# Performance work log

Measured on AMD Instinct MI355X. Metric: run time of the kernel, lower is better.

## Reference

```python
import jax, jax.numpy as jnp
import numpy as np

ROPE_FREQ = 100.0

def _rope1d(tok, pos, freq):
    # tok: [B, H, N, D] (D even), pos: [B, N] int positions
    D = tok.shape[-1]
    inv_freq = 1.0 / (freq ** (jnp.arange(0, D, 2, dtype=jnp.float32) / D))  # [D/2]
    ang = pos[:, None, :, None].astype(jnp.float32) * inv_freq  # [B,1,N,D/2]
    cos = jnp.concatenate([jnp.cos(ang), jnp.cos(ang)], axis=-1).astype(tok.dtype)
    sin = jnp.concatenate([jnp.sin(ang), jnp.sin(ang)], axis=-1).astype(tok.dtype)
    x1, x2 = jnp.split(tok, 2, axis=-1)
    rot = jnp.concatenate([-x2, x1], axis=-1)  # rotate_half
    return tok * cos + rot * sin

def _rope2d(tok, pos2d, freq=ROPE_FREQ):
    # tok: [B, H, N, D]; first half of D encodes y (pos2d[...,0]), second half x (pos2d[...,1])
    y, x = jnp.split(tok, 2, axis=-1)
    y = _rope1d(y, pos2d[..., 0], freq)
    x = _rope1d(x, pos2d[..., 1], freq)
    return jnp.concatenate([y, x], axis=-1)

def setup_inputs() -> dict:
    key = jax.random.key(0)
    B, N, D, Hh = 2, 2048, 768, 12
    ks = jax.random.split(key, 8)
    x = jax.random.normal(ks[0], (B, N, D), dtype=jnp.float32)
    pos2d = jax.random.randint(ks[1], (B, N, 2), 0, 64)
    rope_mask = jax.random.randint(ks[2], (B, N), 0, 2).astype(jnp.bool_)
    s = 1.0 / np.sqrt(D)
    qkv_w = jax.random.normal(ks[3], (3 * D, D), dtype=jnp.float32) * s
    qkv_b = jnp.zeros((3 * D,), dtype=jnp.float32)
    proj_w = jax.random.normal(ks[4], (D, D), dtype=jnp.float32) * s
    proj_b = jnp.zeros((D,), dtype=jnp.float32)
    return {"x": x, "qkv_w": qkv_w, "qkv_b": qkv_b, "proj_w": proj_w,
            "proj_b": proj_b, "pos2d": pos2d, "rope_mask": rope_mask}

def reference(x, qkv_w, qkv_b, proj_w, proj_b, pos2d, rope_mask):
    B, N, C = x.shape
    num_heads = 12
    head_dim = C // num_heads
    scale = head_dim ** -0.5
    qkv = x @ qkv_w.T + qkv_b  # [B,N,3C]
    qkv = qkv.reshape(B, N, 3, num_heads, head_dim).transpose(2, 0, 3, 1, 4)
    q, k, v = qkv[0], qkv[1], qkv[2]  # each [B,H,N,hd]
    q_rope = _rope2d(q, pos2d)
    k_rope = _rope2d(k, pos2d)
    mask = rope_mask[:, None, :, None]  # [B,1,N,1]
    q = jnp.where(mask, q_rope, q)
    k = jnp.where(mask, k_rope, k)
    attn = jnp.einsum('bhqd,bhkd->bhqk', q, k) * scale
    attn = jax.nn.softmax(attn, axis=-1)
    out = jnp.einsum('bhqk,bhkd->bhqd', attn, v)
    out = out.transpose(0, 2, 1, 3).reshape(B, N, C)
    out = out @ proj_w.T + proj_b
    return out
```

## Files before the change

kernel.cpp:

```cpp
#include <hip/hip_runtime.h>
#include <stdint.h>

#define B_  2
#define N_  2048
#define C_  768
#define H_  12
#define NT  (B_*N_)
#define C3  (3*C_)

typedef _Float16 h8 __attribute__((ext_vector_type(8)));
typedef _Float16 h4 __attribute__((ext_vector_type(4)));
typedef float    f4 __attribute__((ext_vector_type(4)));

__device__ __forceinline__ void gload16(const void* g, void* l) {
  __builtin_amdgcn_global_load_lds((const __attribute__((address_space(1))) void*)g,
                                   (__attribute__((address_space(3))) void*)l,
                                   16, 0, 0);
}

__global__ __launch_bounds__(256) void cvt3(const float* __restrict__ x,
                                            const float* __restrict__ w1,
                                            const float* __restrict__ w2,
                                            _Float16* __restrict__ xo,
                                            _Float16* __restrict__ w1o,
                                            _Float16* __restrict__ w2o) {
  const int NX8  = NT*C_/8;
  const int NW18 = C3*C_/8;
  int c = blockIdx.x*256 + threadIdx.x;
  const float* s; _Float16* d; int off;
  if (c < NX8)            { s = x;  d = xo;  off = c; }
  else if (c < NX8+NW18)  { s = w1; d = w1o; off = c - NX8; }
  else                    { s = w2; d = w2o; off = c - NX8 - NW18; }
  f4 a = *(const f4*)(s + (size_t)off*8);
  f4 b = *(const f4*)(s + (size_t)off*8 + 4);
  h8 o;
#pragma unroll
  for (int j = 0; j < 4; ++j) { o[j] = (_Float16)a[j]; o[j+4] = (_Float16)b[j]; }
  *(h8*)(d + (size_t)off*8) = o;
}

__global__ __launch_bounds__(256) void gemm_bt(const _Float16* __restrict__ A,
                                               const _Float16* __restrict__ W,
                                               const float* __restrict__ bias,
                                               _Float16* __restrict__ Ch,
                                               float* __restrict__ Cf,
                                               int M, int N, int K) {
  __shared__ _Float16 Alds[128*32];
  __shared__ _Float16 Wlds[128*32];
  const int tid = threadIdx.x, lane = tid & 63, w = tid >> 6;
  const int m0 = blockIdx.y*128, n0 = blockIdx.x*128;
  const int wm = w >> 1, wn = w & 1;
  const int fr = lane & 15, fq = lane >> 4;

  f4 acc[4][4] = {};

  const int c0 = tid, c1 = tid + 256;
  const _Float16* Ag0 = A + (size_t)(m0 + (c0>>2))*K + (c0&3)*8;
  const _Float16* Ag1 = A + (size_t)(m0 + (c1>>2))*K + (c1&3)*8;
  const _Float16* Wg0 = W + (size_t)(n0 + (c0>>2))*K + (c0&3)*8;
  const _Float16* Wg1 = W + (size_t)(n0 + (c1>>2))*K + (c1&3)*8;
  _Float16* Al0 = Alds + (w*64)*8;
  _Float16* Al1 = Alds + (256 + w*64)*8;
  _Float16* Wl0 = Wlds + (w*64)*8;
  _Float16* Wl1 = Wlds + (256 + w*64)*8;

  for (int kk = 0; kk < K; kk += 32) {
    gload16(Ag0 + kk, Al0);
    gload16(Ag1 + kk, Al1);
    gload16(Wg0 + kk, Wl0);
    gload16(Wg1 + kk, Wl1);
    __syncthreads();
    h8 af[4], wf[4];
#pragma unroll
    for (int mt = 0; mt < 4; ++mt)
      af[mt] = *(const h8*)&Alds[(wm*64 + mt*16 + fr)*32 + fq*8];
#pragma unroll
    for (int nt = 0; nt < 4; ++nt)
      wf[nt] = *(const h8*)&Wlds[(wn*64 + nt*16 + fr)*32 + fq*8];
#pragma unroll
    for (int mt = 0; mt < 4; ++mt)
#pragma unroll
      for (int nt = 0; nt < 4; ++nt)
        acc[mt][nt] = __builtin_amdgcn_mfma_f32_16x16x32_f16(af[mt], wf[nt], acc[mt][nt], 0, 0, 0);
    __syncthreads();
  }

#pragma unroll
  for (int nt = 0; nt < 4; ++nt) {
    const int col = n0 + wn*64 + nt*16 + fr;
    const float bv = bias[col];
#pragma unroll
    for (int mt = 0; mt < 4; ++mt) {
      const int row = m0 + wm*64 + mt*16 + fq*4;
#pragma unroll
      for (int j = 0; j < 4; ++j) {
        const float v = acc[mt][nt][j] + bv;
        if (Ch) Ch[(size_t)(row+j)*N + col] = (_Float16)v;
        else    Cf[(size_t)(row+j)*N + col] = v;
      }
    }
  }
}

__global__ __launch_bounds__(256) void rope_scatter(const _Float16* __restrict__ QKV,
                                                    const int* __restrict__ pos2d,
                                                    const void* __restrict__ maskraw,
                                                    _Float16* __restrict__ Q,
                                                    _Float16* __restrict__ Kd,
                                                    _Float16* __restrict__ Vt) {
  const int tid = threadIdx.x;
  __shared__ int sflags;
  if (tid == 0) sflags = 0;
  __syncthreads();
  const unsigned char* mbytes = (const unsigned char*)maskraw;
  int fl = 0;
#pragma unroll
  for (int k2 = 0; k2 < 16; ++k2) {
    unsigned char v = mbytes[tid*16 + k2];
    if (v == 0x3f) fl |= 1;
    if ((k2 & 3) && v) fl |= 2;
  }
  if (fl) atomicOr(&sflags, fl);
  __syncthreads();
  const int mode = (sflags & 1) ? 2 : ((sflags & 2) ? 1 : 0);

  const int g  = blockIdx.x*256 + tid;
  const int bh = g >> 11;
  const int n  = g & 2047;
  const int b  = bh / H_, h = bh % H_;
  const int t  = b*N_ + n;

  bool msk;
  if (mode == 1)      msk = mbytes[t] != 0;
  else if (mode == 0) msk = ((const int*)maskraw)[t] != 0;
  else                msk = ((const float*)maskraw)[t] != 0.0f;

  const float py = (float)pos2d[t*2 + 0];
  const float px = (float)pos2d[t*2 + 1];

  const _Float16* row = QKV + (size_t)t*C3 + h*64;
  h8 qv[8], kv[8], vv[8];
#pragma unroll
  for (int c = 0; c < 8; ++c) {
    qv[c] = *(const h8*)&row[c*8];
    kv[c] = *(const h8*)&row[C_   + c*8];
    vv[c] = *(const h8*)&row[2*C_ + c*8];
  }
  h8 qo[8], ko[8];
#pragma unroll
  for (int i = 0; i < 16; ++i) {
    const float invf = exp2f((float)i * -0.4152410118f);
    float sy, cy, sx, cx;
    __sincosf(py * invf, &sy, &cy);
    __sincosf(px * invf, &sx, &cx);
    {
      float a = (float)qv[i>>3][i&7], bq = (float)qv[(i+16)>>3][(i+16)&7];
      float r1 = msk ? (a*cy - bq*sy) : a;
      float r2 = msk ? (bq*cy + a*sy) : bq;
      qo[i>>3][i&7]           = (_Float16)(r1 * 0.125f);
      qo[(i+16)>>3][(i+16)&7] = (_Float16)(r2 * 0.125f);
      float ak = (float)kv[i>>3][i&7], bk = (float)kv[(i+16)>>3][(i+16)&7];
      float s1 = msk ? (ak*cy - bk*sy) : ak;
      float s2 = msk ? (bk*cy + ak*sy) : bk;
      ko[i>>3][i&7]           = (_Float16)s1;
      ko[(i+16)>>3][(i+16)&7] = (_Float16)s2;
    }
    {
      float a = (float)qv[(i+32)>>3][(i+32)&7], bq = (float)qv[(i+48)>>3][(i+48)&7];
      float r1 = msk ? (a*cx - bq*sx) : a;
      float r2 = msk ? (bq*cx + a*sx) : bq;
      qo[(i+32)>>3][(i+32)&7] = (_Float16)(r1 * 0.125f);
      qo[(i+48)>>3][(i+48)&7] = (_Float16)(r2 * 0.125f);
      float ak = (float)kv[(i+32)>>3][(i+32)&7], bk = (float)kv[(i+48)>>3][(i+48)&7];
      float s1 = msk ? (ak*cx - bk*sx) : ak;
      float s2 = msk ? (bk*cx + ak*sx) : bk;
      ko[(i+32)>>3][(i+32)&7] = (_Float16)s1;
      ko[(i+48)>>3][(i+48)&7] = (_Float16)s2;
    }
  }
  _Float16* Qrow = Q  + ((size_t)bh*N_ + n)*64;
  _Float16* Krow = Kd + ((size_t)bh*N_ + n)*64;
#pragma unroll
  for (int c = 0; c < 8; ++c) { *(h8*)&Qrow[c*8] = qo[c]; *(h8*)&Krow[c*8] = ko[c]; }
  _Float16* Vb = Vt + (size_t)bh*64*N_ + n;
#pragma unroll
  for (int d = 0; d < 64; ++d) Vb[(size_t)d*N_] = vv[d>>3][d&7];
}

#define KSPLIT 2
__global__ __launch_bounds__(256) void attn(const _Float16* __restrict__ Q,
                                            const _Float16* __restrict__ K,
                                            const _Float16* __restrict__ Vt,
                                            _Float16* __restrict__ Opart,
                                            float* __restrict__ lpart) {
  __shared__ _Float16 Klds[2][64*64];
  __shared__ _Float16 Vlds[2][64*64];
  __shared__ _Float16 Plds[4][32*64];
  const int tid = threadIdx.x, lane = tid & 63, w = tid >> 6;
  const int fr = lane & 15, fq = lane >> 4;
  const int bh = blockIdx.y;
  const int q0 = blockIdx.x * 128;
  const int kb0 = blockIdx.z * (N_/KSPLIT), kb1 = kb0 + N_/KSPLIT;
  const _Float16* Qb = Q  + (size_t)bh*N_*64;
  const _Float16* Kb = K  + (size_t)bh*N_*64;
  const _Float16* Vb = Vt + (size_t)bh*64*N_;

  h8 qf[2][2];
#pragma unroll
  for (int mt = 0; mt < 2; ++mt)
#pragma unroll
    for (int ks = 0; ks < 2; ++ks)
      qf[mt][ks] = *(const h8*)&Qb[(size_t)(q0 + w*32 + mt*16 + fr)*64 + ks*32 + fq*8];

  f4 o[2][4] = {};
  float l_r[2] = {};

  const int sr_l = lane >> 3;
  const int scsw = ((lane & 7) ^ sr_l) * 8;
#define STAGE(buf, kb)                                                          \
  {                                                                             \
    _Float16* kl = &Klds[buf][(w*64)*8];                                        \
    _Float16* vl = &Vlds[buf][(w*64)*8];                                        \
    int r0 = w*8 + sr_l;                                                        \
    gload16(Kb + (size_t)((kb) + r0)*64 + scsw,      kl);                       \
    gload16(Vb + (size_t)r0*N_ + (kb) + scsw,        vl);                       \
    gload16(Kb + (size_t)((kb) + 32 + r0)*64 + scsw, kl + 256*8);               \
    gload16(Vb + (size_t)(32 + r0)*N_ + (kb) + scsw, vl + 256*8);               \
  }

  STAGE(0, kb0);
  int cur = 0;
  const int xm = (fr & 7) << 3;
  _Float16* Pw = &Plds[w][0];

  for (int kb = kb0; kb < kb1; kb += 64) {
    __syncthreads();
    if (kb + 64 < kb1) STAGE(cur^1, kb + 64);

    h8 kf[4][2];
#pragma unroll
    for (int kt = 0; kt < 4; ++kt)
#pragma unroll
      for (int ks = 0; ks < 2; ++ks)
        kf[kt][ks] = *(const h8*)&Klds[cur][(kt*16 + fr)*64 + ((ks*32 + fq*8) ^ xm)];

#pragma unroll
    for (int mt = 0; mt < 2; ++mt) {
      f4 st[4];
#pragma unroll
      for (int kt = 0; kt < 4; ++kt) {
        f4 z = {0.f, 0.f, 0.f, 0.f};
        z      = __builtin_amdgcn_mfma_f32_16x16x32_f16(kf[kt][0], qf[mt][0], z, 0, 0, 0);
        st[kt] = __builtin_amdgcn_mfma_f32_16x16x32_f16(kf[kt][1], qf[mt][1], z, 0, 0, 0);
      }
      const int prow = (mt*16 + fr)*64;
      float lacc = 0.f;
#pragma unroll
      for (int kt = 0; kt < 4; ++kt) {
        float p0 = __builtin_amdgcn_exp2f(__builtin_fmaf(st[kt][0], 1.44269504f, -8.65617025f));
        float p1 = __builtin_amdgcn_exp2f(__builtin_fmaf(st[kt][1], 1.44269504f, -8.65617025f));
        float p2 = __builtin_amdgcn_exp2f(__builtin_fmaf(st[kt][2], 1.44269504f, -8.65617025f));
        float p3 = __builtin_amdgcn_exp2f(__builtin_fmaf(st[kt][3], 1.44269504f, -8.65617025f));
        lacc += (p0 + p1) + (p2 + p3);
        uint2 pk;
        pk.x = __builtin_bit_cast(uint32_t, __builtin_amdgcn_cvt_pkrtz(p0, p1));
        pk.y = __builtin_bit_cast(uint32_t, __builtin_amdgcn_cvt_pkrtz(p2, p3));
        *(uint2*)&Pw[prow + ((kt*16 + fq*4) ^ xm)] = pk;
      }
      l_r[mt] += lacc;
    }

    h8 vf[4][2];
#pragma unroll
    for (int dt = 0; dt < 4; ++dt)
#pragma unroll
      for (int ks = 0; ks < 2; ++ks)
        vf[dt][ks] = *(const h8*)&Vlds[cur][(dt*16 + fr)*64 + ((ks*32 + fq*8) ^ xm)];

#pragma unroll
    for (int mt = 0; mt < 2; ++mt) {
      const int prow = (mt*16 + fr)*64;
      h8 pa0 = *(const h8*)&Pw[prow + ((      fq*8) ^ xm)];
      h8 pa1 = *(const h8*)&Pw[prow + ((32 + fq*8) ^ xm)];
#pragma unroll
      for (int dt = 0; dt < 4; ++dt) {
        o[mt][dt] = __builtin_amdgcn_mfma_f32_16x16x32_f16(vf[dt][0], pa0, o[mt][dt], 0, 0, 0);
        o[mt][dt] = __builtin_amdgcn_mfma_f32_16x16x32_f16(vf[dt][1], pa1, o[mt][dt], 0, 0, 0);
      }
    }
    cur ^= 1;
  }

#pragma unroll
  for (int mt = 0; mt < 2; ++mt) {
    l_r[mt] += __shfl_xor(l_r[mt], 16);
    l_r[mt] += __shfl_xor(l_r[mt], 32);
  }

  _Float16* Ob = Opart + ((size_t)blockIdx.z*24 + bh)*N_*64;
  float*    lb = lpart + ((size_t)blockIdx.z*24 + bh)*N_;
#pragma unroll
  for (int mt = 0; mt < 2; ++mt) {
    const int n = q0 + w*32 + mt*16 + fr;
    if (fq == 0) lb[n] = l_r[mt];
#pragma unroll
    for (int dt = 0; dt < 4; ++dt) {
      h4 ov;
#pragma unroll
      for (int j = 0; j < 4; ++j) ov[j] = (_Float16)o[mt][dt][j];
      *(h4*)&Ob[(size_t)n*64 + dt*16 + fq*4] = ov;
    }
  }
}

__global__ __launch_bounds__(256) void combine(const _Float16* __restrict__ Opart,
                                               const float* __restrict__ lpart,
                                               _Float16* __restrict__ AO) {
  const int g  = blockIdx.x*256 + threadIdx.x;
  const int d8 = g & 7;
  const int n  = (g >> 3) & 2047;
  const int bh = g >> 14;
  const int b = bh / H_, h = bh % H_;
  const size_t r0 = ((size_t)bh*N_ + n);
  const size_t r1 = ((size_t)24*N_ + (size_t)bh*N_ + n);
  h8 o0 = *(const h8*)&Opart[r0*64 + d8*8];
  h8 o1 = *(const h8*)&Opart[r1*64 + d8*8];
  const float inv = 1.0f / (lpart[r0] + lpart[r1]);
  h8 r;
#pragma unroll
  for (int j = 0; j < 8; ++j)
    r[j] = (_Float16)(((float)o0[j] + (float)o1[j]) * inv);
  *(h8*)&AO[((size_t)b*N_ + n)*C_ + h*64 + d8*8] = r;
}

extern "C" void kernel_launch(void* const* d_in, const int* in_sizes, int n_in,
                              void* d_out, int out_size, void* d_ws, size_t ws_size,
                              hipStream_t stream) {
  (void)in_sizes; (void)n_in; (void)out_size; (void)ws_size;
  const float* x      = (const float*)d_in[0];
  const float* qkv_w  = (const float*)d_in[1];
  const float* qkv_b  = (const float*)d_in[2];
  const float* proj_w = (const float*)d_in[3];
  const float* proj_b = (const float*)d_in[4];
  const int*   pos2d  = (const int*)d_in[5];
  const void*  rmask  = d_in[6];
  float* out = (float*)d_out;
  char* ws = (char*)d_ws;

  _Float16* Wqh   = (_Float16*)(ws + 0);
  _Float16* Wph   = (_Float16*)(ws + 3538944);
  _Float16* Kh    = (_Float16*)(ws + 4718592);
  _Float16* Vth   = (_Float16*)(ws + 11010048);
  _Float16* Xh    = (_Float16*)(ws + 17301504);
  _Float16* QKVh  = (_Float16*)(ws + 23592960);
  _Float16* Qh    = Xh;
  _Float16* Opart = (_Float16*)(ws + 23592960);
  float*    lpart = (float*)(ws + 36175872);
  _Float16* AOh   = Xh;

  cvt3<<<2688, 256, 0, stream>>>(x, qkv_w, proj_w, Xh, Wqh, Wph);
  gemm_bt<<<dim3(C3/128, NT/128), 256, 0, stream>>>(Xh, Wqh, qkv_b, QKVh, nullptr, NT, C3, C_);
  rope_scatter<<<(B_*H_*N_)/256, 256, 0, stream>>>(QKVh, pos2d, rmask, Qh, Kh, Vth);
  attn<<<dim3(N_/128, B_*H_, KSPLIT), 256, 0, stream>>>(Qh, Kh, Vth, Opart, lpart);
  combine<<<(24*N_*8)/256, 256, 0, stream>>>(Opart, lpart, AOh);
  gemm_bt<<<dim3(C_/128, NT/128), 256, 0, stream>>>(AOh, Wph, proj_b, nullptr, out, NT, C_, C_);
}
```

Before: 123.2 us.

## Switch attention to 32x32x16 MFMA and keep P in registers via lane shuffles

Rewrites the attention inner loop to use 32x32x16 f16 MFMA tiles instead of 16x16x32. The probability tile is no longer round-tripped through LDS: it is packed to fp16 and rearranged across half-waves with shuffles so it can feed the PV MFMA directly as the B operand. Plds shared memory goes away and launch bounds now ask for 3 blocks per CU, which should raise occupancy and cut LDS traffic. In exchange the shuffle and select logic is more intricate, and the larger accumulators may increase register pressure.

```diff
diff --git a/kernel.cpp b/kernel.cpp
--- a/kernel.cpp
+++ b/kernel.cpp
@@ -11,6 +11,8 @@
 typedef _Float16 h8 __attribute__((ext_vector_type(8)));
 typedef _Float16 h4 __attribute__((ext_vector_type(4)));
 typedef float    f4 __attribute__((ext_vector_type(4)));
+typedef float    f16x __attribute__((ext_vector_type(16)));
+typedef uint32_t u4 __attribute__((ext_vector_type(4)));
 
 __device__ __forceinline__ void gload16(const void* g, void* l) {
   __builtin_amdgcn_global_load_lds((const __attribute__((address_space(1))) void*)g,
@@ -188,16 +190,17 @@
 }
 
 #define KSPLIT 2
-__global__ __launch_bounds__(256) void attn(const _Float16* __restrict__ Q,
-                                            const _Float16* __restrict__ K,
-                                            const _Float16* __restrict__ Vt,
-                                            _Float16* __restrict__ Opart,
-                                            float* __restrict__ lpart) {
+__global__ __launch_bounds__(256, 3) void attn(const _Float16* __restrict__ Q,
+                                               const _Float16* __restrict__ K,
+                                               const _Float16* __restrict__ Vt,
+                                               _Float16* __restrict__ Opart,
+                                               float* __restrict__ lpart) {
   __shared__ _Float16 Klds[2][64*64];
   __shared__ _Float16 Vlds[2][64*64];
-  __shared__ _Float16 Plds[4][32*64];
   const int tid = threadIdx.x, lane = tid & 63, w = tid >> 6;
-  const int fr = lane & 15, fq = lane >> 4;
+  const int q32 = lane & 31;
+  const int hi  = lane >> 5;
+  const bool ishi = hi != 0;
   const int bh = blockIdx.y;
   const int q0 = blockIdx.x * 128;
   const int kb0 = blockIdx.z * (N_/KSPLIT), kb1 = kb0 + N_/KSPLIT;
@@ -205,15 +208,17 @@
   const _Float16* Kb = K  + (size_t)bh*N_*64;
   const _Float16* Vb = Vt + (size_t)bh*64*N_;
 
-  h8 qf[2][2];
-#pragma unroll
-  for (int mt = 0; mt < 2; ++mt)
-#pragma unroll
-    for (int ks = 0; ks < 2; ++ks)
-      qf[mt][ks] = *(const h8*)&Qb[(size_t)(q0 + w*32 + mt*16 + fr)*64 + ks*32 + fq*8];
-
-  f4 o[2][4] = {};
-  float l_r[2] = {};
+  h8 qf[4];
+#pragma unroll
+  for (int s = 0; s < 4; ++s)
+    qf[s] = *(const h8*)&Qb[(size_t)(q0 + w*32 + q32)*64 + s*16 + hi*8];
+
+  f16x o[2];
+#pragma unroll
+  for (int dg = 0; dg < 2; ++dg)
+#pragma unroll
+    for (int r = 0; r < 16; ++r) o[dg][r] = 0.f;
+  float l_r = 0.f;
 
   const int sr_l = lane >> 3;
   const int scsw = ((lane & 7) ^ sr_l) * 8;
@@ -230,87 +235,74 @@
 
   STAGE(0, kb0);
   int cur = 0;
-  const int xm = (fr & 7) << 3;
-  _Float16* Pw = &Plds[w][0];
+  const int xr = (q32 & 7) << 3;
 
   for (int kb = kb0; kb < kb1; kb += 64) {
     __syncthreads();
     if (kb + 64 < kb1) STAGE(cur^1, kb + 64);
 
-    h8 kf[4][2];
-#pragma unroll
-    for (int kt = 0; kt < 4; ++kt)
-#pragma unroll
-      for (int ks = 0; ks < 2; ++ks)
-        kf[kt][ks] = *(const h8*)&Klds[cur][(kt*16 + fr)*64 + ((ks*32 + fq*8) ^ xm)];
-
-#pragma unroll
-    for (int mt = 0; mt < 2; ++mt) {
-      f4 st[4];
-#pragma unroll
-      for (int kt = 0; kt < 4; ++kt) {
-        f4 z = {0.f, 0.f, 0.f, 0.f};
-        z      = __builtin_amdgcn_mfma_f32_16x16x32_f16(kf[kt][0], qf[mt][0], z, 0, 0, 0);
-        st[kt] = __builtin_amdgcn_mfma_f32_16x16x32_f16(kf[kt][1], qf[mt][1], z, 0, 0, 0);
+#pragma unroll
+    for (int kg = 0; kg < 2; ++kg) {
+      f16x st;
+#pragma unroll
+      for (int r = 0; r < 16; ++r) st[r] = 0.f;
+#pragma unroll
+      for (int s = 0; s < 4; ++s) {
+        h8 kf = *(const h8*)&Klds[cur][(kg*32 + q32)*64 + ((s*16 + hi*8) ^ xr)];
+        st = __builtin_amdgcn_mfma_f32_32x32x16_f16(kf, qf[s], st, 0, 0, 0);
       }
-      const int prow = (mt*16 + fr)*64;
+      float p[16];
       float lacc = 0.f;
 #pragma unroll
-      for (int kt = 0; kt < 4; ++kt) {
-        float p0 = __builtin_amdgcn_exp2f(__builtin_fmaf(st[kt][0], 1.44269504f, -8.65617025f));
-        float p1 = __builtin_amdgcn_exp2f(__builtin_fmaf(st[kt][1], 1.44269504f, -8.65617025f));
-        float p2 = __builtin_amdgcn_exp2f(__builtin_fmaf(st[kt][2], 1.44269504f, -8.65617025f));
-        float p3 = __builtin_amdgcn_exp2f(__builtin_fmaf(st[kt][3], 1.44269504f, -8.65617025f));
-        lacc += (p0 + p1) + (p2 + p3);
-        uint2 pk;
-        pk.x = __builtin_bit_cast(uint32_t, __builtin_amdgcn_cvt_pkrtz(p0, p1));
-        pk.y = __builtin_bit_cast(uint32_t, __builtin_amdgcn_cvt_pkrtz(p2, p3));
-        *(uint2*)&Pw[prow + ((kt*16 + fq*4) ^ xm)] = pk;
+      for (int r = 0; r < 16; ++r) {
+        p[r] = __builtin_amdgcn_exp2f(__builtin_fmaf(st[r], 1.44269504f, -8.65617025f));
+        lacc += p[r];
       }
-      l_r[mt] += lacc;
-    }
-
-    h8 vf[4][2];
-#pragma unroll
-    for (int dt = 0; dt < 4; ++dt)
-#pragma unroll
-      for (int ks = 0; ks < 2; ++ks)
-        vf[dt][ks] = *(const h8*)&Vlds[cur][(dt*16 + fr)*64 + ((ks*32 + fq*8) ^ xm)];
-
-#pragma unroll
-    for (int mt = 0; mt < 2; ++mt) {
-      const int prow = (mt*16 + fr)*64;
-      h8 pa0 = *(const h8*)&Pw[prow + ((      fq*8) ^ xm)];
-      h8 pa1 = *(const h8*)&Pw[prow + ((32 + fq*8) ^ xm)];
-#pragma unroll
-      for (int dt = 0; dt < 4; ++dt) {
-        o[mt][dt] = __builtin_amdgcn_mfma_f32_16x16x32_f16(vf[dt][0], pa0, o[mt][dt], 0, 0, 0);
-        o[mt][dt] = __builtin_amdgcn_mfma_f32_16x16x32_f16(vf[dt][1], pa1, o[mt][dt], 0, 0, 0);
+      l_r += lacc;
+      uint32_t dd[8];
+#pragma unroll
+      for (int m = 0; m < 8; ++m)
+        dd[m] = __builtin_bit_cast(uint32_t, __builtin_amdgcn_cvt_pkrtz(p[2*m], p[2*m+1]));
+#pragma unroll
+      for (int s16 = 0; s16 < 2; ++s16) {
+        uint32_t K1 = ishi ? dd[4*s16+2] : dd[4*s16+0];
+        uint32_t K2 = ishi ? dd[4*s16+3] : dd[4*s16+1];
+        uint32_t S1 = ishi ? dd[4*s16+0] : dd[4*s16+2];
+        uint32_t S2 = ishi ? dd[4*s16+1] : dd[4*s16+3];
+        uint32_t Y1 = (uint32_t)__shfl_xor((int)S1, 32);
+        uint32_t Y2 = (uint32_t)__shfl_xor((int)S2, 32);
+        u4 bb;
+        bb[0] = ishi ? Y1 : K1;
+        bb[1] = ishi ? Y2 : K2;
+        bb[2] = ishi ? K1 : Y1;
+        bb[3] = ishi ? K2 : Y2;
+        h8 pb = __builtin_bit_cast(h8, bb);
+        const int kcol = kg*32 + s16*16 + hi*8;
+#pragma unroll
+        for (int dg = 0; dg < 2; ++dg) {
+          h8 vf = *(const h8*)&Vlds[cur][(dg*32 + q32)*64 + (kcol ^ xr)];
+          o[dg] = __builtin_amdgcn_mfma_f32_32x32x16_f16(vf, pb, o[dg], 0, 0, 0);
+        }
       }
     }
     cur ^= 1;
   }
 
-#pragma unroll
-  for (int mt = 0; mt < 2; ++mt) {
-    l_r[mt] += __shfl_xor(l_r[mt], 16);
-    l_r[mt] += __shfl_xor(l_r[mt], 32);
-  }
+  l_r += __shfl_xor(l_r, 32);
 
   _Float16* Ob = Opart + ((size_t)blockIdx.z*24 + bh)*N_*64;
   float*    lb = lpart + ((size_t)blockIdx.z*24 + bh)*N_;
-#pragma unroll
-  for (int mt = 0; mt < 2; ++mt) {
-    const int n = q0 + w*32 + mt*16 + fr;
-    if (fq == 0) lb[n] = l_r[mt];
-#pragma unroll
-    for (int dt = 0; dt < 4; ++dt) {
+  const int n = q0 + w*32 + q32;
+  if (!ishi) lb[n] = l_r;
+#pragma unroll
+  for (int dg = 0; dg < 2; ++dg)
+#pragma unroll
+    for (int rq = 0; rq < 4; ++rq) {
       h4 ov;
 #pragma unroll
-      for (int j = 0; j < 4; ++j) ov[j] = (_Float16)o[mt][dt][j];
-      *(h4*)&Ob[(size_t)n*64 + dt*16 + fq*4] = ov;
-    }
-  }
+      for (int j = 0; j < 4; ++j) ov[j] = (_Float16)o[dg][rq*4 + j];
+      *(h4*)&Ob[(size_t)n*64 + dg*32 + rq*8 + hi*4] = ov;
+    }
 }
 
 __global__ __launch_bounds__(256) void combine(const _Float16* __restrict__ Opart,
```

After: 123.3 us. Within noise of the previous version (+0.1%).
